# Optimization experiments

Hardware: AMD Instinct MI355X
Metric: run time of the kernel (lower is better)

Reference implementation:

```python
import jax, jax.numpy as jnp
import numpy as np

BN_EPS = 1e-5


def _attention(x, fc_w, bn_g, bn_b, bn_m, bn_v, ch_w, ch_b, fl_w, fl_b, sp_w, sp_b):
    # x: (B, C, H, W). Returns channel (B,C), filter (B,C), spatial (B,1,1,3,3) attentions.
    p = jnp.mean(x, axis=(2, 3))                                  # global avg pool -> (B, C)
    y = p @ fc_w.T                                                # 1x1 conv == matmul -> (B, A)
    y = (y - bn_m) / jnp.sqrt(bn_v + BN_EPS) * bn_g + bn_b        # BatchNorm (eval / running stats)
    y = jax.nn.relu(y)
    ch = jax.nn.sigmoid(y @ ch_w.T + ch_b)                        # channel attention (B, C_in)
    fl = jax.nn.sigmoid(y @ fl_w.T + fl_b)                        # filter attention (B, C_out)
    sp = jax.nn.sigmoid(y @ sp_w.T + sp_b).reshape(-1, 1, 1, 3, 3)  # spatial attention
    return ch, fl, sp


def _conv_same(x, w):
    # x: (N, Cin, H, W), w: (Cout, Cin, kh, kw), stride 1, padding 1 (SAME for 3x3)
    return jax.lax.conv_general_dilated(x, w, (1, 1), 'SAME',
                                        dimension_numbers=('NCHW', 'OIHW', 'NCHW'))


def _dynamic_conv(xb, wb):
    # per-sample conv: xb (C,H,W), wb (Cout,Cin,3,3)
    return _conv_same(xb[None], wb)[0]


def reference(x, od_weight, fc_w, bn_g, bn_b, bn_m, bn_v, ch_w, ch_b,
              fl_w, fl_b, sp_w, sp_b, conv2_w, conv2_b):
    ch, fl, sp = _attention(x, fc_w, bn_g, bn_b, bn_m, bn_v,
                            ch_w, ch_b, fl_w, fl_b, sp_w, sp_b)
    xw = x * ch[:, :, None, None]                                 # channel attention on input
    # kernel_num=1 -> kernel attention is identity; aggregate weight per sample:
    w = sp * od_weight[None]                                      # (B, Cout, Cin, 3, 3)
    y = jax.vmap(_dynamic_conv)(xw, w)                            # ODConv output (B, Cout, H, W)
    y = y * fl[:, :, None, None]                                  # filter attention on output
    y = _conv_same(y, conv2_w) + conv2_b[None, :, None, None]     # plain 3x3 conv
    y = jax.nn.gelu(y, approximate=False)                         # nn.GELU (exact erf)
    return x + y                                                  # residual


def setup_inputs() -> dict:
    key = jax.random.key(0)
    ks = jax.random.split(key, 8)
    B, C, H, W, A = 8, 128, 192, 192, 16
    s_in = 1.0 / np.sqrt(C * 9)
    s_a = 1.0 / np.sqrt(A)
    return {
        'x': jax.random.normal(ks[0], (B, C, H, W), jnp.float32),
        'od_weight': jax.random.normal(ks[1], (C, C, 3, 3), jnp.float32) * s_in,
        'fc_w': jax.random.normal(ks[2], (A, C), jnp.float32) / np.sqrt(C),
        'bn_g': jnp.ones((A,), jnp.float32),
        'bn_b': jnp.zeros((A,), jnp.float32),
        'bn_m': jnp.zeros((A,), jnp.float32),
        'bn_v': jnp.ones((A,), jnp.float32),
        'ch_w': jax.random.normal(ks[3], (C, A), jnp.float32) * s_a,
        'ch_b': jnp.zeros((C,), jnp.float32),
        'fl_w': jax.random.normal(ks[4], (C, A), jnp.float32) * s_a,
        'fl_b': jnp.zeros((C,), jnp.float32),
        'sp_w': jax.random.normal(ks[5], (9, A), jnp.float32) * s_a,
        'sp_b': jnp.zeros((9,), jnp.float32),
        'conv2_w': jax.random.normal(ks[6], (C, C, 3, 3), jnp.float32) * s_in,
        'conv2_b': jnp.zeros((C,), jnp.float32),
    }
```

## Files before the change

### kernel.cpp

```cpp
#include <hip/hip_runtime.h>
#include <math.h>

typedef short bf16x8 __attribute__((ext_vector_type(8)));
typedef float f32x4 __attribute__((ext_vector_type(4)));
typedef unsigned short u16;
typedef unsigned int u32;

#define BB 8
#define C_IN 128
#define HH 192
#define WW 192
#define A_DIM 16
#define HW_ (192 * 192)

__device__ __forceinline__ u16 f2b(float f) {
    u32 u = __float_as_uint(f);
    return (u16)((u + 0x7fffu + ((u >> 16) & 1u)) >> 16);
}
__device__ __forceinline__ float b2f(u16 u) {
    return __uint_as_float(((u32)u) << 16);
}

__global__ void avgpool_kernel(const float* __restrict__ x, float* __restrict__ p) {
    int bc = blockIdx.x;
    const float4* xp = (const float4*)(x + (size_t)bc * HW_);
    float s = 0.f;
    for (int i = threadIdx.x; i < HW_ / 4; i += 256) {
        float4 v = xp[i];
        s += v.x + v.y + v.z + v.w;
    }
    for (int off = 32; off; off >>= 1) s += __shfl_down(s, off, 64);
    __shared__ float red[4];
    int lane = threadIdx.x & 63, wid = threadIdx.x >> 6;
    if (lane == 0) red[wid] = s;
    __syncthreads();
    if (threadIdx.x == 0)
        p[bc] = (red[0] + red[1] + red[2] + red[3]) * (1.0f / HW_);
}

__global__ void attention_kernel(const float* __restrict__ p,
                                 const float* __restrict__ fc_w,
                                 const float* __restrict__ bn_g, const float* __restrict__ bn_b,
                                 const float* __restrict__ bn_m, const float* __restrict__ bn_v,
                                 const float* __restrict__ ch_w, const float* __restrict__ ch_b,
                                 const float* __restrict__ fl_w, const float* __restrict__ fl_b,
                                 const float* __restrict__ sp_w, const float* __restrict__ sp_b,
                                 float* __restrict__ ch, float* __restrict__ fl,
                                 float* __restrict__ sp) {
    __shared__ float pl[BB * C_IN];
    __shared__ float yl[BB * A_DIM];
    int t = threadIdx.x;
    for (int i = t; i < BB * C_IN; i += 256) pl[i] = p[i];
    __syncthreads();
    if (t < BB * A_DIM) {
        int b = t / A_DIM, a = t % A_DIM;
        float s = 0.f;
        for (int c = 0; c < C_IN; ++c) s += pl[b * C_IN + c] * fc_w[a * C_IN + c];
        s = (s - bn_m[a]) * rsqrtf(bn_v[a] + 1e-5f) * bn_g[a] + bn_b[a];
        yl[t] = fmaxf(s, 0.f);
    }
    __syncthreads();
    for (int idx = t; idx < BB * C_IN; idx += 256) {
        int b = idx / C_IN, c = idx % C_IN;
        float s1 = ch_b[c], s2 = fl_b[c];
        for (int a = 0; a < A_DIM; ++a) {
            float yv = yl[b * A_DIM + a];
            s1 += yv * ch_w[c * A_DIM + a];
            s2 += yv * fl_w[c * A_DIM + a];
        }
        ch[idx] = 1.f / (1.f + expf(-s1));
        fl[idx] = 1.f / (1.f + expf(-s2));
    }
    if (t < BB * 9) {
        int b = t / 9, k = t % 9;
        float s = sp_b[k];
        for (int a = 0; a < A_DIM; ++a) s += yl[b * A_DIM + a] * sp_w[k * A_DIM + a];
        sp[t] = 1.f / (1.f + expf(-s));
    }
}

__global__ void prep_w(const float* __restrict__ od, const float* __restrict__ w2,
                       const float* __restrict__ ch, const float* __restrict__ fl,
                       const float* __restrict__ sp,
                       u16* __restrict__ wp, u16* __restrict__ w2p) {
    int t = blockIdx.x * 256 + threadIdx.x;
    int ii = t % 40;
    int r = t / 40;
    int o = r % 128; r /= 128;
    int ic = r & 3;
    int bidx = r >> 2;
    size_t cbase = (size_t)(ic * 9) * 5120 + o * 40 + ii;
    u16* dst = (bidx < 8) ? (wp + (size_t)bidx * 184320 + cbase) : (w2p + cbase);
    if (ii >= 32) {
#pragma unroll
        for (int tap = 0; tap < 9; ++tap) dst[(size_t)tap * 5120] = 0;
        return;
    }
    int i = ic * 32 + ii;
    if (bidx < 8) {
        float s = fl[bidx * 128 + o] * ch[bidx * 128 + i];
#pragma unroll
        for (int tap = 0; tap < 9; ++tap) {
            float v = od[((size_t)o * 128 + i) * 9 + tap] * s * sp[bidx * 9 + tap];
            dst[(size_t)tap * 5120] = f2b(v);
        }
    } else {
#pragma unroll
        for (int tap = 0; tap < 9; ++tap)
            dst[(size_t)tap * 5120] = f2b(w2[((size_t)o * 128 + i) * 9 + tap]);
    }
}

template <bool EPI, bool SBF>
__global__ __launch_bounds__(256, 3) void convk(const void* __restrict__ srcv,
                                                const u16* __restrict__ wgl,
                                                const float* __restrict__ bias,
                                                const float* __restrict__ xres,
                                                void* __restrict__ dstv) {
    __shared__ __align__(16) u16 xbuf[2][4][180][8];
    __shared__ __align__(16) u16 wbuf[2][5120];

    const int tid = threadIdx.x;
    const int lane = tid & 63;
    const int wid = tid >> 6;
    const int lcol = lane & 15, klane = lane >> 4;
    const int wave_m = wid >> 1, wave_n = wid & 1;
    const int tile = blockIdx.x, b = blockIdx.y;
    const int h0 = (tile / 12) * 8, w0 = (tile % 12) * 16;

    const char* wsrc = (const char*)(EPI ? wgl : (wgl + (size_t)b * 184320));

    float xr[3][8];

    auto stageW = [&](int phase) {
        const char* g = wsrc + (size_t)phase * 10240;
        char* l = (char*)&wbuf[phase & 1][0];
#pragma unroll
        for (int r = 0; r < 3; ++r) {
            int off = (wid + r * 4) << 10;
            if (off < 10240)
                __builtin_amdgcn_global_load_lds(
                    (const __attribute__((address_space(1))) void*)(g + off + lane * 16),
                    (__attribute__((address_space(3))) void*)(l + off), 16, 0, 0);
        }
    };
    auto stageXload = [&](int c) {
#pragma unroll
        for (int it = 0; it < 3; ++it) {
            int idx = tid + it * 256;
            if (idx < 720) {
                int g = idx / 180, pp = idx - g * 180;
                int gh = h0 - 1 + pp / 18, gw = w0 - 1 + pp % 18;
                bool ok = ((unsigned)gh < 192u) && ((unsigned)gw < 192u);
#pragma unroll
                for (int j = 0; j < 8; ++j) {
                    float v = 0.f;
                    if (ok) {
                        size_t a = (((size_t)b * 128 + c * 32 + g * 8 + j) * 192 + gh) * 192 + gw;
                        v = SBF ? b2f(((const u16*)srcv)[a]) : ((const float*)srcv)[a];
                    }
                    xr[it][j] = v;
                }
            }
        }
    };
    auto stageXwrite = [&](int buf) {
#pragma unroll
        for (int it = 0; it < 3; ++it) {
            int idx = tid + it * 256;
            if (idx < 720) {
                int g = idx / 180, pp = idx - g * 180;
                union { u16 u[8]; uint4 v; } pk;
#pragma unroll
                for (int j = 0; j < 8; ++j) pk.u[j] = f2b(xr[it][j]);
                *(uint4*)&xbuf[buf][g][pp][0] = pk.v;
            }
        }
    };

    f32x4 acc[4][4];
#pragma unroll
    for (int m = 0; m < 4; ++m)
#pragma unroll
        for (int n = 0; n < 4; ++n) acc[m][n] = (f32x4){0.f, 0.f, 0.f, 0.f};

    stageXload(0);
    stageW(0);
    stageXwrite(0);
    __syncthreads();

    for (int ic = 0; ic < 4; ++ic) {
        if (ic < 3) stageXload(ic + 1);
#pragma unroll
        for (int tap = 0; tap < 9; ++tap) {
            const int phase = ic * 9 + tap;
            if (phase + 1 < 36) stageW(phase + 1);
            const int dh = tap / 3, dw = tap % 3;
            bf16x8 af[4], bfr[4];
            const u16* wb_ = &wbuf[(ic + tap) & 1][0];
#pragma unroll
            for (int m = 0; m < 4; ++m)
                af[m] = *(const bf16x8*)&wb_[(wave_m * 64 + m * 16 + lcol) * 40 + klane * 8];
#pragma unroll
            for (int n = 0; n < 4; ++n) {
                int pp = (wave_n * 4 + n + dh) * 18 + lcol + dw;
                bfr[n] = *(const bf16x8*)&xbuf[ic & 1][klane][pp][0];
            }
#pragma unroll
            for (int m = 0; m < 4; ++m)
#pragma unroll
                for (int n = 0; n < 4; ++n)
                    acc[m][n] = __builtin_amdgcn_mfma_f32_16x16x32_bf16(af[m], bfr[n],
                                                                        acc[m][n], 0, 0, 0);
            if (tap == 8 && ic < 3) stageXwrite((ic + 1) & 1);
            __syncthreads();
        }
    }

#pragma unroll
    for (int m = 0; m < 4; ++m) {
        const int o = wave_m * 64 + m * 16 + klane * 4;
#pragma unroll
        for (int n = 0; n < 4; ++n) {
            const int h = h0 + wave_n * 4 + n;
            const int w = w0 + lcol;
            size_t base = (((size_t)b * 128 + o) * 192 + h) * 192 + w;
#pragma unroll
            for (int r = 0; r < 4; ++r) {
                float v = acc[m][n][r];
                size_t adr = base + (size_t)r * HW_;
                if (EPI) {
                    v += bias[o + r];
                    float ge = 0.5f * v * (1.f + erff(v * 0.70710678118654752f));
                    ((float*)dstv)[adr] = xres[adr] + ge;
                } else {
                    ((u16*)dstv)[adr] = f2b(v);
                }
            }
        }
    }
}

extern "C" void kernel_launch(void* const* d_in, const int* in_sizes, int n_in,
                              void* d_out, int out_size, void* d_ws, size_t ws_size,
                              hipStream_t stream) {
    const float* x       = (const float*)d_in[0];
    const float* od      = (const float*)d_in[1];
    const float* fc_w    = (const float*)d_in[2];
    const float* bn_g    = (const float*)d_in[3];
    const float* bn_b    = (const float*)d_in[4];
    const float* bn_m    = (const float*)d_in[5];
    const float* bn_v    = (const float*)d_in[6];
    const float* ch_w    = (const float*)d_in[7];
    const float* ch_b    = (const float*)d_in[8];
    const float* fl_w    = (const float*)d_in[9];
    const float* fl_b    = (const float*)d_in[10];
    const float* sp_w    = (const float*)d_in[11];
    const float* sp_b    = (const float*)d_in[12];
    const float* conv2_w = (const float*)d_in[13];
    const float* conv2_b = (const float*)d_in[14];
    float* out = (float*)d_out;

    char* wsb = (char*)d_ws;
    u16* y1  = (u16*)wsb;
    u16* wp  = (u16*)(wsb + 75497472);
    u16* w2p = (u16*)(wsb + 75497472 + 2949120);
    float* pbuf = (float*)(wsb + 75497472 + 2949120 + 368640);
    float* chb  = pbuf + 1024;
    float* flb  = chb + 1024;
    float* spb  = flb + 1024;

    avgpool_kernel<<<1024, 256, 0, stream>>>(x, pbuf);
    attention_kernel<<<1, 256, 0, stream>>>(pbuf, fc_w, bn_g, bn_b, bn_m, bn_v,
                                            ch_w, ch_b, fl_w, fl_b, sp_w, sp_b,
                                            chb, flb, spb);
    prep_w<<<720, 256, 0, stream>>>(od, conv2_w, chb, flb, spb, wp, w2p);
    convk<false, false><<<dim3(288, 8), 256, 0, stream>>>(x, wp, nullptr, nullptr, y1);
    convk<true, true><<<dim3(288, 8), 256, 0, stream>>>(y1, w2p, conv2_b, x, out);
}
```

Measured before the change: 690.5 us.

## Deepen weight prefetch to 4 stages with MFMA-fragment layout and vmcnt waits

The packed weight layout changes from padded rows (stride 40) to MFMA-fragment order, so each lane reads a contiguous 16-byte fragment and the padding bytes disappear. The conv kernel now keeps a 4-slot weight ring with loads issued three phases ahead and a single X buffer. Full __syncthreads are replaced by explicit vmcnt waits plus s_barrier, and MFMA issue priority is raised. X halo loads are clamped so they run unconditionally. The risks are subtle sync errors from the hand-counted waitcnt values and possible LDS bank conflicts in the new layout.

New measurement: 686.9 us. About the same (-0.5%).

```diff
diff --git a/kernel.cpp b/kernel.cpp
--- a/kernel.cpp
+++ b/kernel.cpp
@@ -84,32 +84,37 @@
                        const float* __restrict__ sp,
                        u16* __restrict__ wp, u16* __restrict__ w2p) {
     int t = blockIdx.x * 256 + threadIdx.x;
-    int ii = t % 40;
-    int r = t / 40;
-    int o = r % 128; r /= 128;
-    int ic = r & 3;
-    int bidx = r >> 2;
-    size_t cbase = (size_t)(ic * 9) * 5120 + o * 40 + ii;
-    u16* dst = (bidx < 8) ? (wp + (size_t)bidx * 184320 + cbase) : (w2p + cbase);
-    if (ii >= 32) {
-#pragma unroll
-        for (int tap = 0; tap < 9; ++tap) dst[(size_t)tap * 5120] = 0;
-        return;
-    }
-    int i = ic * 32 + ii;
+    int kl = t & 3;
+    int q = t >> 2;
+    int o = q & 127; q >>= 7;
+    int tap = q % 9; q /= 9;
+    int ic = q & 3;
+    int bidx = q >> 2;
+
+    u16* base = (bidx < 8) ? (wp + (size_t)bidx * 147456) : w2p;
+    u16* dst = base + (size_t)(ic * 9 + tap) * 4096 +
+               (size_t)((o >> 4) * 64 + kl * 16 + (o & 15)) * 8;
+
+    union { u16 u[8]; uint4 v; } pk;
     if (bidx < 8) {
-        float s = fl[bidx * 128 + o] * ch[bidx * 128 + i];
-#pragma unroll
-        for (int tap = 0; tap < 9; ++tap) {
-            float v = od[((size_t)o * 128 + i) * 9 + tap] * s * sp[bidx * 9 + tap];
-            dst[(size_t)tap * 5120] = f2b(v);
+        float s = fl[bidx * 128 + o] * sp[bidx * 9 + tap];
+#pragma unroll
+        for (int j = 0; j < 8; ++j) {
+            int i = ic * 32 + kl * 8 + j;
+            float v = od[((size_t)o * 128 + i) * 9 + tap] * s * ch[bidx * 128 + i];
+            pk.u[j] = f2b(v);
         }
     } else {
 #pragma unroll
-        for (int tap = 0; tap < 9; ++tap)
-            dst[(size_t)tap * 5120] = f2b(w2[((size_t)o * 128 + i) * 9 + tap]);
-    }
-}
+        for (int j = 0; j < 8; ++j) {
+            int i = ic * 32 + kl * 8 + j;
+            pk.u[j] = f2b(w2[((size_t)o * 128 + i) * 9 + tap]);
+        }
+    }
+    *(uint4*)dst = pk.v;
+}
+
+#define WAITV(N) asm volatile("s_waitcnt vmcnt(" #N ")" ::: "memory")
 
 template <bool EPI, bool SBF>
 __global__ __launch_bounds__(256, 3) void convk(const void* __restrict__ srcv,
@@ -117,8 +122,8 @@
                                                 const float* __restrict__ bias,
                                                 const float* __restrict__ xres,
                                                 void* __restrict__ dstv) {
-    __shared__ __align__(16) u16 xbuf[2][4][180][8];
-    __shared__ __align__(16) u16 wbuf[2][5120];
+    __shared__ __align__(16) u16 xbuf[4][180][8];
+    __shared__ __align__(16) u16 wbuf[4][4096];
 
     const int tid = threadIdx.x;
     const int lane = tid & 63;
@@ -128,23 +133,23 @@
     const int tile = blockIdx.x, b = blockIdx.y;
     const int h0 = (tile / 12) * 8, w0 = (tile % 12) * 16;
 
-    const char* wsrc = (const char*)(EPI ? wgl : (wgl + (size_t)b * 184320));
+    const char* wsrc = (const char*)(EPI ? wgl : (wgl + (size_t)b * 147456));
 
     float xr[3][8];
 
-    auto stageW = [&](int phase) {
-        const char* g = wsrc + (size_t)phase * 10240;
-        char* l = (char*)&wbuf[phase & 1][0];
-#pragma unroll
-        for (int r = 0; r < 3; ++r) {
-            int off = (wid + r * 4) << 10;
-            if (off < 10240)
-                __builtin_amdgcn_global_load_lds(
-                    (const __attribute__((address_space(1))) void*)(g + off + lane * 16),
-                    (__attribute__((address_space(3))) void*)(l + off), 16, 0, 0);
-        }
+    auto issueW = [&](int p) {
+        const char* g = wsrc + (size_t)p * 8192;
+        char* l = (char*)&wbuf[p & 3][0];
+        int off = wid << 10;
+        __builtin_amdgcn_global_load_lds(
+            (const __attribute__((address_space(1))) void*)(g + off + lane * 16),
+            (__attribute__((address_space(3))) void*)(l + off), 16, 0, 0);
+        off += 4096;
+        __builtin_amdgcn_global_load_lds(
+            (const __attribute__((address_space(1))) void*)(g + off + lane * 16),
+            (__attribute__((address_space(3))) void*)(l + off), 16, 0, 0);
     };
-    auto stageXload = [&](int c) {
+    auto loadX = [&](int c) {
 #pragma unroll
         for (int it = 0; it < 3; ++it) {
             int idx = tid + it * 256;
@@ -152,19 +157,17 @@
                 int g = idx / 180, pp = idx - g * 180;
                 int gh = h0 - 1 + pp / 18, gw = w0 - 1 + pp % 18;
                 bool ok = ((unsigned)gh < 192u) && ((unsigned)gw < 192u);
+                int ghc = min(max(gh, 0), 191), gwc = min(max(gw, 0), 191);
 #pragma unroll
                 for (int j = 0; j < 8; ++j) {
-                    float v = 0.f;
-                    if (ok) {
-                        size_t a = (((size_t)b * 128 + c * 32 + g * 8 + j) * 192 + gh) * 192 + gw;
-                        v = SBF ? b2f(((const u16*)srcv)[a]) : ((const float*)srcv)[a];
-                    }
-                    xr[it][j] = v;
+                    size_t a = (((size_t)b * 128 + c * 32 + g * 8 + j) * 192 + ghc) * 192 + gwc;
+                    float v = SBF ? b2f(((const u16*)srcv)[a]) : ((const float*)srcv)[a];
+                    xr[it][j] = ok ? v : 0.f;
                 }
             }
         }
     };
-    auto stageXwrite = [&](int buf) {
+    auto writeX = [&]() {
 #pragma unroll
         for (int it = 0; it < 3; ++it) {
             int idx = tid + it * 256;
@@ -173,7 +176,7 @@
                 union { u16 u[8]; uint4 v; } pk;
 #pragma unroll
                 for (int j = 0; j < 8; ++j) pk.u[j] = f2b(xr[it][j]);
-                *(uint4*)&xbuf[buf][g][pp][0] = pk.v;
+                *(uint4*)&xbuf[g][pp][0] = pk.v;
             }
         }
     };
@@ -184,36 +187,63 @@
 #pragma unroll
         for (int n = 0; n < 4; ++n) acc[m][n] = (f32x4){0.f, 0.f, 0.f, 0.f};
 
-    stageXload(0);
-    stageW(0);
-    stageXwrite(0);
-    __syncthreads();
-
-    for (int ic = 0; ic < 4; ++ic) {
-        if (ic < 3) stageXload(ic + 1);
-#pragma unroll
-        for (int tap = 0; tap < 9; ++tap) {
-            const int phase = ic * 9 + tap;
-            if (phase + 1 < 36) stageW(phase + 1);
-            const int dh = tap / 3, dw = tap % 3;
+    loadX(0);
+    asm volatile("" ::: "memory");
+    issueW(0); issueW(1); issueW(2);
+    WAITV(4);
+    writeX();
+    asm volatile("s_waitcnt lgkmcnt(0)" ::: "memory");
+    __builtin_amdgcn_sched_barrier(0);
+    __builtin_amdgcn_s_barrier();
+
+#pragma unroll
+    for (int c = 0; c < 4; ++c) {
+#pragma unroll
+        for (int t = 0; t < 9; ++t) {
+            const int p = c * 9 + t;
+            const int dh = t / 3, dw = t % 3;
+
             bf16x8 af[4], bfr[4];
-            const u16* wb_ = &wbuf[(ic + tap) & 1][0];
+            const u16* wb_ = &wbuf[p & 3][0];
 #pragma unroll
             for (int m = 0; m < 4; ++m)
-                af[m] = *(const bf16x8*)&wb_[(wave_m * 64 + m * 16 + lcol) * 40 + klane * 8];
+                af[m] = *(const bf16x8*)&wb_[(size_t)((wave_m * 4 + m) * 64 + lane) * 8];
 #pragma unroll
             for (int n = 0; n < 4; ++n) {
                 int pp = (wave_n * 4 + n + dh) * 18 + lcol + dw;
-                bfr[n] = *(const bf16x8*)&xbuf[ic & 1][klane][pp][0];
-            }
+                bfr[n] = *(const bf16x8*)&xbuf[klane][pp][0];
+            }
+
+            if (p + 3 < 36) issueW(p + 3);
+            if (t == 5 && c < 3) {
+                asm volatile("" ::: "memory");
+                loadX(c + 1);
+            }
+
+            __builtin_amdgcn_s_setprio(1);
 #pragma unroll
             for (int m = 0; m < 4; ++m)
 #pragma unroll
                 for (int n = 0; n < 4; ++n)
                     acc[m][n] = __builtin_amdgcn_mfma_f32_16x16x32_bf16(af[m], bfr[n],
                                                                         acc[m][n], 0, 0, 0);
-            if (tap == 8 && ic < 3) stageXwrite((ic + 1) & 1);
-            __syncthreads();
+            __builtin_amdgcn_s_setprio(0);
+
+            if (p <= 34) {
+                const int xl = (c < 3 && (t == 5 || t == 6 || t == 7)) ? 24 : 0;
+                const int wn = ((p <= 33) ? 2 : 0) + ((p <= 32) ? 2 : 0) + xl;
+                if (wn == 28) WAITV(28);
+                else if (wn == 4) WAITV(4);
+                else if (wn == 2) WAITV(2);
+                else WAITV(0);
+            }
+            if (p < 35) __builtin_amdgcn_s_barrier();
+            if (t == 8 && c < 3) {
+                writeX();
+                asm volatile("s_waitcnt lgkmcnt(0)" ::: "memory");
+                __builtin_amdgcn_sched_barrier(0);
+                __builtin_amdgcn_s_barrier();
+            }
         }
     }
 
@@ -264,8 +294,8 @@
     char* wsb = (char*)d_ws;
     u16* y1  = (u16*)wsb;
     u16* wp  = (u16*)(wsb + 75497472);
-    u16* w2p = (u16*)(wsb + 75497472 + 2949120);
-    float* pbuf = (float*)(wsb + 75497472 + 2949120 + 368640);
+    u16* w2p = (u16*)(wsb + 75497472 + 2359296);
+    float* pbuf = (float*)(wsb + 75497472 + 2359296 + 294912);
     float* chb  = pbuf + 1024;
     float* flb  = chb + 1024;
     float* spb  = flb + 1024;
@@ -274,7 +304,7 @@
     attention_kernel<<<1, 256, 0, stream>>>(pbuf, fc_w, bn_g, bn_b, bn_m, bn_v,
                                             ch_w, ch_b, fl_w, fl_b, sp_w, sp_b,
                                             chb, flb, spb);
-    prep_w<<<720, 256, 0, stream>>>(od, conv2_w, chb, flb, spb, wp, w2p);
+    prep_w<<<648, 256, 0, stream>>>(od, conv2_w, chb, flb, spb, wp, w2p);
     convk<false, false><<<dim3(288, 8), 256, 0, stream>>>(x, wp, nullptr, nullptr, y1);
     convk<true, true><<<dim3(288, 8), 256, 0, stream>>>(y1, w2p, conv2_b, x, out);
 }
```
